# Optimization experiments

Measured on AMD Instinct MI355X. Metric: run time of the kernel, lower is better.

Reference implementation:

```python
import jax, jax.numpy as jnp
import numpy as np

N_NODES = 100000
N_EDGES = 20000
NNZ = 1000000
IN_CH = 128
OUT_DIM = 64  # heads(8) * out_channels(8)


def setup_inputs() -> dict:
    key = jax.random.key(0)
    k1, k2, k3, k4, k5, k6 = jax.random.split(key, 6)
    X = jax.random.normal(k1, (N_NODES, IN_CH), dtype=jnp.float32)
    vertex = jax.random.randint(k2, (NNZ,), 0, N_NODES, dtype=jnp.int64)
    edges = jax.random.randint(k3, (NNZ,), 0, N_EDGES, dtype=jnp.int64)
    W_lin = jax.random.normal(k4, (IN_CH, OUT_DIM), dtype=jnp.float32) * (1.0 / np.sqrt(IN_CH))
    degE = jax.random.uniform(k5, (N_EDGES, 1), dtype=jnp.float32)
    degV = jax.random.uniform(k6, (N_NODES, 1), dtype=jnp.float32)
    W_edge = jnp.ones((N_EDGES, 1), dtype=jnp.float32)
    return {"X": X, "vertex": vertex, "edges": edges, "W_lin": W_lin,
            "degE": degE, "degV": degV, "W_edge": W_edge}


def reference(X, vertex, edges, W_lin, degE, degV, W_edge):
    # linear projection (no bias): [N, in] @ [in, heads*out] -> [N, D]
    Xl = X @ W_lin
    # gather node features per incidence, scatter-sum into hyperedges
    Xve = Xl[vertex]                                             # [nnz, D]
    Xe = jax.ops.segment_sum(Xve, edges, num_segments=N_EDGES)   # [E, D]
    Xe = Xe * degE * W_edge                                      # edge degree + weight scaling
    # gather hyperedge features per incidence, scatter-sum back to nodes
    Xev = Xe[edges]                                              # [nnz, D]
    Xv = jax.ops.segment_sum(Xev, vertex, num_segments=N_NODES)  # [N, D]
    return Xv * degV
```

## Files before the change

kernel.cpp:

```cpp
#include <hip/hip_runtime.h>
#include <hip/hip_bf16.h>

typedef __hip_bfloat16 bf16;
__device__ __forceinline__ float bf2f(bf16 v) { return __bfloat162float(v); }

typedef __attribute__((ext_vector_type(8))) short short8;
typedef __attribute__((ext_vector_type(4))) float floatx4;

#define EB_BITS 8
#define VB_BITS 10
#define MAXBK   256
#define F1_ITEMS 2048
#define XS_STRIDE 136
#define SMEM_INTS 5892
#define HF_MAXIT 20

__device__ __forceinline__ int rbase(int b, int nEB, int capE, int capV) {
  return (b < nEB) ? b * capE : nEB * capE + (b - nEB) * capV;
}

__global__ void init_cursor_kernel(int* __restrict__ gcursor, int KB,
                                   int nEB, int capE, int capV) {
  const int b = threadIdx.x;
  if (b < KB) gcursor[b] = rbase(b, nEB, capE, capV);
}

__device__ void bucketize_body(int* smem4,
    const int* __restrict__ vertex, const int* __restrict__ edges,
    int* __restrict__ gcursor, int* __restrict__ records,
    int nnz, int KB, int nEB, int bb) {
  int* cnt    = smem4;
  int* scanEx = smem4 + 256;
  int* bases  = smem4 + 512;
  int* wsum4  = smem4 + 768;
  int* staged = smem4 + 772;
  unsigned char* sbkt = (unsigned char*)(smem4 + 772 + 4096);

  const int tid  = threadIdx.x;
  const int lane = tid & 63;
  const int wid  = tid >> 6;
  const int base = bb * F1_ITEMS;
  const int iEnd = min(nnz, base + F1_ITEMS);

  cnt[tid] = 0;
  __syncthreads();

  int recs[16], bks[16], ps[16];
#pragma unroll
  for (int j = 0; j < 8; ++j) {
    const int i = base + tid + j * 256;
    if (i < iEnd) {
      const int e = __builtin_nontemporal_load(&edges[i]);
      const int v = __builtin_nontemporal_load(&vertex[i]);
      const int bkE = e >> EB_BITS;
      const int bkV = nEB + (v >> VB_BITS);
      recs[2*j]   = ((e & ((1 << EB_BITS) - 1)) << 17) | v;
      bks[2*j]    = bkE;
      ps[2*j]     = atomicAdd(&cnt[bkE], 1);
      recs[2*j+1] = ((v & ((1 << VB_BITS) - 1)) << 17) | e;
      bks[2*j+1]  = bkV;
      ps[2*j+1]   = atomicAdd(&cnt[bkV], 1);
    } else {
      bks[2*j] = -1;  bks[2*j+1] = -1;
    }
  }
  __syncthreads();

  const int c = cnt[tid];
  int inc = c;
#pragma unroll
  for (int d = 1; d < 64; d <<= 1) {
    int t = __shfl_up(inc, d, 64);
    if (lane >= d) inc += t;
  }
  if (lane == 63) wsum4[wid] = inc;
  __syncthreads();
  if (tid < 4) {
    int wv = wsum4[tid];
#pragma unroll
    for (int d = 1; d < 4; d <<= 1) {
      int t = __shfl_up(wv, d, 64);
      if (tid >= d) wv += t;
    }
    wsum4[tid] = wv;
  }
  __syncthreads();
  const int excl = inc - c + (wid > 0 ? wsum4[wid - 1] : 0);

  if (tid < KB && c > 0) bases[tid] = atomicAdd(&gcursor[tid], c);
  scanEx[tid] = excl;
  __syncthreads();

#pragma unroll
  for (int j = 0; j < 16; ++j) {
    if (bks[j] >= 0) {
      const int s = scanEx[bks[j]] + ps[j];
      staged[s] = recs[j];
      sbkt[s] = (unsigned char)bks[j];
    }
  }
  __syncthreads();

  const int nrec = 2 * (iEnd - base);
  for (int s = tid; s < nrec; s += 256) {
    const int b = sbkt[s];
    records[bases[b] + (s - scanEx[b])] = staged[s];
  }
}

__device__ __forceinline__ unsigned int pack_bf16x2(float lo, float hi) {
  bf16 a = __float2bfloat16(lo);
  bf16 b = __float2bfloat16(hi);
  unsigned short ua = *(unsigned short*)&a;
  unsigned short ub = *(unsigned short*)&b;
  return (unsigned int)ua | ((unsigned int)ub << 16);
}

__device__ void gemm_body(int* smem4,
    const float* __restrict__ X, const float* __restrict__ W,
    bf16* __restrict__ Xl, int Nrows, int ntiles, int gb, int GB) {
  unsigned short* S = (unsigned short*)smem4;

  const int tid  = threadIdx.x;
  const int wave = tid >> 6;
  const int lane = tid & 63;
  const int quad = lane >> 4;
  const int l15  = lane & 15;

  for (int i = tid; i < 8192; i += 256) {
    const int k = i >> 6, n = i & 63;
    bf16 h = __float2bfloat16(W[i]);
    S[n * XS_STRIDE + k] = *(unsigned short*)&h;
  }
  __syncthreads();

  short8 bfrag[4][4];
#pragma unroll
  for (int ct = 0; ct < 4; ++ct)
#pragma unroll
    for (int kt = 0; kt < 4; ++kt)
      bfrag[ct][kt] = *(const short8*)&S[(ct * 16 + l15) * XS_STRIDE + kt * 32 + quad * 8];
  __syncthreads();

  const int r  = tid >> 2;
  const int c0 = (tid & 3) * 32;

  for (int tile = gb; tile < ntiles; tile += GB) {
    const int row0 = tile * 64;
    {
      int rr = row0 + r;
      if (rr >= Nrows) rr = Nrows - 1;
      const float* src = X + (size_t)rr * 128 + c0;
      unsigned short* dst = &S[r * XS_STRIDE + c0];
#pragma unroll
      for (int q = 0; q < 4; ++q) {
        const float4 f0 = *(const float4*)(src + q * 8);
        const float4 f1 = *(const float4*)(src + q * 8 + 4);
        uint4 o;
        o.x = pack_bf16x2(f0.x, f0.y);
        o.y = pack_bf16x2(f0.z, f0.w);
        o.z = pack_bf16x2(f1.x, f1.y);
        o.w = pack_bf16x2(f1.z, f1.w);
        *(uint4*)(dst + q * 8) = o;
      }
    }
    __syncthreads();

    const int m = wave * 16 + l15;
    short8 afrag[4];
#pragma unroll
    for (int kt = 0; kt < 4; ++kt)
      afrag[kt] = *(const short8*)&S[m * XS_STRIDE + kt * 32 + quad * 8];

    floatx4 acc[4];
#pragma unroll
    for (int ct = 0; ct < 4; ++ct) {
      acc[ct] = (floatx4){0.f, 0.f, 0.f, 0.f};
#pragma unroll
      for (int kt = 0; kt < 4; ++kt)
        acc[ct] = __builtin_amdgcn_mfma_f32_16x16x32_bf16(
            afrag[kt], bfrag[ct][kt], acc[ct], 0, 0, 0);
    }

    const int rbase_ = row0 + wave * 16 + quad * 4;
#pragma unroll
    for (int ct = 0; ct < 4; ++ct) {
      const int col = ct * 16 + l15;
#pragma unroll
      for (int reg = 0; reg < 4; ++reg) {
        const int row = rbase_ + reg;
        if (row < Nrows) Xl[(size_t)row * 64 + col] = __float2bfloat16(acc[ct][reg]);
      }
    }
    __syncthreads();
  }
}

__global__ __launch_bounds__(256) void fused1_kernel(
    const int* __restrict__ vertex, const int* __restrict__ edges,
    int* __restrict__ gcursor, int* __restrict__ records,
    const float* __restrict__ X, const float* __restrict__ W,
    bf16* __restrict__ Xl,
    int nnz, int KB, int nEB, int Nrows, int ntiles, int GB) {
  __shared__ int smem4[SMEM_INTS];
  if ((int)blockIdx.x < GB)
    gemm_body(smem4, X, W, Xl, Nrows, ntiles, blockIdx.x, GB);
  else
    bucketize_body(smem4, vertex, edges, gcursor, records, nnz, KB, nEB,
                   blockIdx.x - GB);
}

__global__ __launch_bounds__(1024) void histfill_kernel(
    const int* __restrict__ records, const int* __restrict__ gcursor,
    int* __restrict__ offs, int* __restrict__ perm,
    int nEB, int capE, int capV, int E, int M, int KB, int totrec) {
  __shared__ int cnt[1 << VB_BITS];
  __shared__ int wsum[16];
  const int b    = blockIdx.x;
  const int tid  = threadIdx.x;
  const int lane = tid & 63;
  const int wid  = tid >> 6;

  const int base = rbase(b, nEB, capE, capV);
  const int end  = gcursor[b];

  int bb = 0;
  {
    const int tot = (tid < KB) ? (gcursor[tid] - rbase(tid, nEB, capE, capV)) : 0;
    int inc = tot;
    if (tid < 256) {
#pragma unroll
      for (int d = 1; d < 64; d <<= 1) {
        const int t = __shfl_up(inc, d, 64);
        if (lane >= d) inc += t;
      }
      if (lane == 63) wsum[wid] = inc;
    }
    __syncthreads();
    if (tid < 256) {
      int wbase = 0;
      for (int w = 0; w < wid; ++w) wbase += wsum[w];
      cnt[tid] = wbase + inc - tot;
    }
    __syncthreads();
    bb = cnt[b];
    __syncthreads();
  }
  if (b == 0 && tid == 0) offs[M] = totrec;

  cnt[tid] = 0;
  __syncthreads();

  int myrec[HF_MAXIT], myp[HF_MAXIT];
#pragma unroll
  for (int it = 0; it < HF_MAXIT; ++it) {
    const int r = base + tid + it * 1024;
    if (r < end) {
      const int rec = __builtin_nontemporal_load(&records[r]);
      myrec[it] = rec;
      myp[it] = atomicAdd(&cnt[rec >> 17], 1);
    } else {
      myrec[it] = -1;
    }
  }
  __syncthreads();

  const int c = cnt[tid];
  int inc = c;
#pragma unroll
  for (int d = 1; d < 64; d <<= 1) {
    const int t = __shfl_up(inc, d, 64);
    if (lane >= d) inc += t;
  }
  if (lane == 63) wsum[wid] = inc;
  __syncthreads();
  if (tid < 16) {
    int wv = wsum[tid];
#pragma unroll
    for (int d = 1; d < 16; d <<= 1) {
      const int t = __shfl_up(wv, d, 64);
      if (tid >= d) wv += t;
    }
    wsum[tid] = wv;
  }
  __syncthreads();
  const int goff = bb + inc - c + (wid > 0 ? wsum[wid - 1] : 0);

  int seg_lo, segN;
  if (b < nEB) { seg_lo = b << EB_BITS;               segN = min(E - seg_lo, 1 << EB_BITS); }
  else         { seg_lo = E + ((b - nEB) << VB_BITS); segN = min(M - seg_lo, 1 << VB_BITS); }
  if (tid < segN) offs[seg_lo + tid] = goff;
  cnt[tid] = goff;
  __syncthreads();

#pragma unroll
  for (int it = 0; it < HF_MAXIT; ++it) {
    if (myrec[it] >= 0)
      perm[cnt[myrec[it] >> 17] + myp[it]] = myrec[it] & 0x1FFFF;
  }
}

__global__ __launch_bounds__(256) void gather_e_kernel(
    const bf16* __restrict__ Xl, const int* __restrict__ perm,
    const int* __restrict__ offs, const float* __restrict__ degE,
    const float* __restrict__ W_edge, bf16* __restrict__ Xe, int E) {
  const int gtid = blockIdx.x * 256 + threadIdx.x;
  const int e    = gtid >> 6;
  const int lane = gtid & 63;
  if (e >= E) return;

  const int beg = offs[e];
  const int end = offs[e + 1];
  float acc = 0.f;

  for (int base = beg; base < end; base += 64) {
    const int n = min(64, end - base);
    const int idx = (lane < n) ? perm[base + lane] : 0;
    int jj = 0;
    for (; jj + 4 <= n; jj += 4) {
      const int v0 = __shfl(idx, jj + 0, 64);
      const int v1 = __shfl(idx, jj + 1, 64);
      const int v2 = __shfl(idx, jj + 2, 64);
      const int v3 = __shfl(idx, jj + 3, 64);
      const float f0 = bf2f(Xl[(size_t)v0 * 64 + lane]);
      const float f1 = bf2f(Xl[(size_t)v1 * 64 + lane]);
      const float f2 = bf2f(Xl[(size_t)v2 * 64 + lane]);
      const float f3 = bf2f(Xl[(size_t)v3 * 64 + lane]);
      acc += (f0 + f1) + (f2 + f3);
    }
    for (; jj < n; ++jj) {
      const int v = __shfl(idx, jj, 64);
      acc += bf2f(Xl[(size_t)v * 64 + lane]);
    }
  }
  const float s = degE[e] * W_edge[e];
  Xe[(size_t)e * 64 + lane] = __float2bfloat16(acc * s);
}

__global__ __launch_bounds__(256) void gather_v_kernel(
    const bf16* __restrict__ Xe, const int* __restrict__ perm,
    const int* __restrict__ offs, const float* __restrict__ degV,
    float* __restrict__ out, int N, int E) {
  const int gtid = blockIdx.x * 256 + threadIdx.x;
  const int v    = gtid >> 6;
  const int lane = gtid & 63;
  if (v >= N) return;

  const int beg = offs[E + v];
  const int end = offs[E + v + 1];
  float acc = 0.f;

  for (int base = beg; base < end; base += 64) {
    const int n = min(64, end - base);
    const int idx = (lane < n) ? perm[base + lane] : 0;
    int jj = 0;
    for (; jj + 4 <= n; jj += 4) {
      const int e0 = __shfl(idx, jj + 0, 64);
      const int e1 = __shfl(idx, jj + 1, 64);
      const int e2 = __shfl(idx, jj + 2, 64);
      const int e3 = __shfl(idx, jj + 3, 64);
      const float f0 = bf2f(Xe[(size_t)e0 * 64 + lane]);
      const float f1 = bf2f(Xe[(size_t)e1 * 64 + lane]);
      const float f2 = bf2f(Xe[(size_t)e2 * 64 + lane]);
      const float f3 = bf2f(Xe[(size_t)e3 * 64 + lane]);
      acc += (f0 + f1) + (f2 + f3);
    }
    for (; jj < n; ++jj) {
      const int e = __shfl(idx, jj, 64);
      acc += bf2f(Xe[(size_t)e * 64 + lane]);
    }
  }
  __builtin_nontemporal_store(acc * degV[v], &out[(size_t)v * 64 + lane]);
}

extern "C" void kernel_launch(void* const* d_in, const int* in_sizes, int n_in,
                              void* d_out, int out_size, void* d_ws, size_t ws_size,
                              hipStream_t stream) {
  const float* X      = (const float*)d_in[0];
  const int*   vertex = (const int*)d_in[1];
  const int*   edges  = (const int*)d_in[2];
  const float* W      = (const float*)d_in[3];
  const float* degE   = (const float*)d_in[4];
  const float* degV   = (const float*)d_in[5];
  const float* W_edge = (const float*)d_in[6];
  float* out = (float*)d_out;

  const int nnz = in_sizes[1];
  const int E   = in_sizes[4];
  const int N   = in_sizes[5];
  const int M   = E + N;

  const int nEB = (E + (1 << EB_BITS) - 1) >> EB_BITS;
  const int nVB = (N + (1 << VB_BITS) - 1) >> VB_BITS;
  const int KB  = nEB + nVB;

  int capE = (nnz / nEB) * 3 / 2 + 256;
  int capV = (nnz / nVB) * 3 / 2 + 256;
  if (capE > HF_MAXIT * 1024) capE = HF_MAXIT * 1024;
  if (capV > HF_MAXIT * 1024) capV = HF_MAXIT * 1024;
  const size_t rec_total = (size_t)nEB * capE + (size_t)nVB * capV;

  char* p = (char*)d_ws;
  auto alloc = [&](size_t bytes) -> void* {
    void* r = (void*)p;
    p += (bytes + 255) & ~(size_t)255;
    return r;
  };
  int*  offs    = (int*)alloc((size_t)(M + 1) * 4);
  int*  gcursor = (int*)alloc(MAXBK * 4);
  int*  perm    = (int*)alloc((size_t)2 * nnz * 4);
  int*  records = (int*)alloc(rec_total * 4);
  bf16* Xl      = (bf16*)alloc((size_t)N * 64 * 2);
  bf16* Xe      = (bf16*)alloc((size_t)E * 64 * 2);

  const int f1blocks = (nnz + F1_ITEMS - 1) / F1_ITEMS;
  const int ntiles   = (N + 63) / 64;
  const int GB       = ntiles < 512 ? ntiles : 512;

  init_cursor_kernel<<<1, MAXBK, 0, stream>>>(gcursor, KB, nEB, capE, capV);
  fused1_kernel<<<GB + f1blocks, 256, 0, stream>>>(
      vertex, edges, gcursor, records, X, W, Xl,
      nnz, KB, nEB, N, ntiles, GB);
  histfill_kernel<<<KB, 1024, 0, stream>>>(records, gcursor, offs, perm,
                                           nEB, capE, capV, E, M, KB, 2 * nnz);
  gather_e_kernel<<<(E + 3) / 4, 256, 0, stream>>>(Xl, perm, offs, degE, W_edge, Xe, E);
  gather_v_kernel<<<(N + 3) / 4, 256, 0, stream>>>(Xe, perm, offs, degV, out, N, E);
}
```

Baseline: 113.7 us.

## Split histfill by bucket type and overlap vertex histfill with edge gather

The histfill kernel is split into an edge-bucket launch and a combined launch in which vertex-bucket histfill blocks run alongside the edge gather blocks, which now use 1024-thread blocks. The goal is to overlap the vertex CSR construction with the edge aggregation and to drop one kernel launch. The cursor-init kernel becomes a memset, with cursors now holding relative counts and the region base added at use. The edge-range sentinel offs[E] is written early so the gather can run before the vertex histfill finishes, which needs careful reasoning about ordering.

```diff
diff --git a/kernel.cpp b/kernel.cpp
--- a/kernel.cpp
+++ b/kernel.cpp
@@ -19,16 +19,10 @@
   return (b < nEB) ? b * capE : nEB * capE + (b - nEB) * capV;
 }
 
-__global__ void init_cursor_kernel(int* __restrict__ gcursor, int KB,
-                                   int nEB, int capE, int capV) {
-  const int b = threadIdx.x;
-  if (b < KB) gcursor[b] = rbase(b, nEB, capE, capV);
-}
-
 __device__ void bucketize_body(int* smem4,
     const int* __restrict__ vertex, const int* __restrict__ edges,
     int* __restrict__ gcursor, int* __restrict__ records,
-    int nnz, int KB, int nEB, int bb) {
+    int nnz, int KB, int nEB, int capE, int capV, int bb) {
   int* cnt    = smem4;
   int* scanEx = smem4 + 256;
   int* bases  = smem4 + 512;
@@ -87,7 +81,8 @@
   __syncthreads();
   const int excl = inc - c + (wid > 0 ? wsum4[wid - 1] : 0);
 
-  if (tid < KB && c > 0) bases[tid] = atomicAdd(&gcursor[tid], c);
+  if (tid < KB && c > 0)
+    bases[tid] = rbase(tid, nEB, capE, capV) + atomicAdd(&gcursor[tid], c);
   scanEx[tid] = excl;
   __syncthreads();
 
@@ -201,32 +196,32 @@
     int* __restrict__ gcursor, int* __restrict__ records,
     const float* __restrict__ X, const float* __restrict__ W,
     bf16* __restrict__ Xl,
-    int nnz, int KB, int nEB, int Nrows, int ntiles, int GB) {
+    int nnz, int KB, int nEB, int capE, int capV, int Nrows, int ntiles, int GB) {
   __shared__ int smem4[SMEM_INTS];
   if ((int)blockIdx.x < GB)
     gemm_body(smem4, X, W, Xl, Nrows, ntiles, blockIdx.x, GB);
   else
     bucketize_body(smem4, vertex, edges, gcursor, records, nnz, KB, nEB,
-                   blockIdx.x - GB);
-}
-
-__global__ __launch_bounds__(1024) void histfill_kernel(
+                   capE, capV, blockIdx.x - GB);
+}
+
+__device__ void histfill_body(
     const int* __restrict__ records, const int* __restrict__ gcursor,
     int* __restrict__ offs, int* __restrict__ perm,
-    int nEB, int capE, int capV, int E, int M, int KB, int totrec) {
+    int b, int nEB, int capE, int capV, int E, int M, int KB, int totrec,
+    bool sentinel) {
   __shared__ int cnt[1 << VB_BITS];
   __shared__ int wsum[16];
-  const int b    = blockIdx.x;
   const int tid  = threadIdx.x;
   const int lane = tid & 63;
   const int wid  = tid >> 6;
 
   const int base = rbase(b, nEB, capE, capV);
-  const int end  = gcursor[b];
+  const int end  = base + gcursor[b];
 
   int bb = 0;
   {
-    const int tot = (tid < KB) ? (gcursor[tid] - rbase(tid, nEB, capE, capV)) : 0;
+    const int tot = (tid < KB) ? gcursor[tid] : 0;
     int inc = tot;
     if (tid < 256) {
 #pragma unroll
@@ -244,9 +239,12 @@
     }
     __syncthreads();
     bb = cnt[b];
+    if (sentinel) {
+      if (tid == 0)   offs[M] = totrec;
+      if (tid == nEB) offs[E] = cnt[nEB];
+    }
     __syncthreads();
   }
-  if (b == 0 && tid == 0) offs[M] = totrec;
 
   cnt[tid] = 0;
   __syncthreads();
@@ -300,13 +298,29 @@
   }
 }
 
-__global__ __launch_bounds__(256) void gather_e_kernel(
-    const bf16* __restrict__ Xl, const int* __restrict__ perm,
-    const int* __restrict__ offs, const float* __restrict__ degE,
-    const float* __restrict__ W_edge, bf16* __restrict__ Xe, int E) {
-  const int gtid = blockIdx.x * 256 + threadIdx.x;
-  const int e    = gtid >> 6;
-  const int lane = gtid & 63;
+__global__ __launch_bounds__(1024) void histfill_e_kernel(
+    const int* __restrict__ records, const int* __restrict__ gcursor,
+    int* __restrict__ offs, int* __restrict__ perm,
+    int nEB, int capE, int capV, int E, int M, int KB, int totrec) {
+  histfill_body(records, gcursor, offs, perm, blockIdx.x,
+                nEB, capE, capV, E, M, KB, totrec, blockIdx.x == 0);
+}
+
+__global__ __launch_bounds__(1024) void hfv_ge_kernel(
+    const int* __restrict__ records, const int* __restrict__ gcursor,
+    int* __restrict__ offs, int* __restrict__ perm,
+    const bf16* __restrict__ Xl, const float* __restrict__ degE,
+    const float* __restrict__ W_edge, bf16* __restrict__ Xe,
+    int nEB, int nVB, int capE, int capV, int E, int M, int KB, int totrec) {
+  const int bid = blockIdx.x;
+  if (bid < nVB) {
+    histfill_body(records, gcursor, offs, perm, nEB + bid,
+                  nEB, capE, capV, E, M, KB, totrec, false);
+    return;
+  }
+  const int tid  = threadIdx.x;
+  const int lane = tid & 63;
+  const int e    = (bid - nVB) * 16 + (tid >> 6);
   if (e >= E) return;
 
   const int beg = offs[e];
@@ -416,13 +430,16 @@
   const int f1blocks = (nnz + F1_ITEMS - 1) / F1_ITEMS;
   const int ntiles   = (N + 63) / 64;
   const int GB       = ntiles < 512 ? ntiles : 512;
-
-  init_cursor_kernel<<<1, MAXBK, 0, stream>>>(gcursor, KB, nEB, capE, capV);
+  const int geb      = (E + 15) / 16;
+
+  hipMemsetAsync(gcursor, 0, MAXBK * 4, stream);
   fused1_kernel<<<GB + f1blocks, 256, 0, stream>>>(
       vertex, edges, gcursor, records, X, W, Xl,
-      nnz, KB, nEB, N, ntiles, GB);
-  histfill_kernel<<<KB, 1024, 0, stream>>>(records, gcursor, offs, perm,
-                                           nEB, capE, capV, E, M, KB, 2 * nnz);
-  gather_e_kernel<<<(E + 3) / 4, 256, 0, stream>>>(Xl, perm, offs, degE, W_edge, Xe, E);
+      nnz, KB, nEB, capE, capV, N, ntiles, GB);
+  histfill_e_kernel<<<nEB, 1024, 0, stream>>>(records, gcursor, offs, perm,
+                                              nEB, capE, capV, E, M, KB, 2 * nnz);
+  hfv_ge_kernel<<<nVB + geb, 1024, 0, stream>>>(records, gcursor, offs, perm,
+                                                Xl, degE, W_edge, Xe,
+                                                nEB, nVB, capE, capV, E, M, KB, 2 * nnz);
   gather_v_kernel<<<(N + 3) / 4, 256, 0, stream>>>(Xe, perm, offs, degV, out, N, E);
 }
```

After: 129.8 us. 14.2% more time.
